# Optimization experiments

Hardware: AMD Instinct MI355X
Metric: run time of the kernel (lower is better)

The kernel has to match this reference:

```python
import jax, jax.numpy as jnp
import numpy as np

N_CONN = 21  # n_connections


def setup_inputs() -> dict:
    key = jax.random.key(0)
    landmarks = jax.random.normal(key, (262144, N_CONN, 3), dtype=jnp.float32)
    return {"landmarks": landmarks}


def reference(landmarks) -> jnp.ndarray:
    # Faithful to the TF layer: connections = [(i, j) for i in range(n) for j in range(n)],
    # connection_vectors[k] = landmarks[:, j_k] - landmarks[:, i_k]; the loop only reads
    # indices k < n, which correspond to pairs (0, k), so v_k = p_k - p_0 (v_0 == 0).
    b, n = landmarks.shape[0], N_CONN
    v = landmarks[:, :n, :] - landmarks[:, :1, :]          # (b, n, d)
    dots = jnp.einsum("bid,bjd->bij", v, v)                 # (b, n, n)
    norms = jnp.linalg.norm(v, axis=-1)                     # (b, n)
    cos = dots / (norms[:, :, None] * norms[:, None, :])    # 0/0 -> nan for v_0
    ang = jnp.arccos(cos)                                   # (b, n, n)
    ang = jnp.where(jnp.isnan(ang), jnp.zeros_like(ang), ang)
    # TF concatenates n*n tensors of shape (batch,) along axis -1 (== axis 0),
    # yielding shape (n*n*batch,) ordered angle-major.
    return ang.reshape(b, n * n).T.reshape(-1)
```

## Files before the change

### kernel.cpp

```cpp
#include <hip/hip_runtime.h>

#define NCONN 21

typedef float f4 __attribute__((ext_vector_type(4)));

__device__ __forceinline__ float acos_poly(float c) {
    c = fmaxf(fminf(c, 1.0f), -1.0f);
    float t = fabsf(c);
    float s = sqrtf(1.0f - t);
    float p = fmaf(t, -0.0187293f, 0.0742610f);
    p = fmaf(t, p, -0.2121144f);
    p = fmaf(t, p, 1.5707288f);
    float r = s * p;
    return (c >= 0.0f) ? r : (3.14159265358979f - r);
}

__global__ __launch_bounds__(256, 2) void k1_planes(const float* __restrict__ in,
                                                    float* __restrict__ ws, int B) {
    __shared__ float lds[256 * 64];
    const int tid = threadIdx.x;
    const long long blockBatch = (long long)blockIdx.x * 256;

    const long long gBase4 = blockBatch * 63 / 4;
    const float4* in4 = (const float4*)in;
    #pragma unroll
    for (int it = 0; it < 16; ++it) {
        int t4 = tid + it * 256;
        if (t4 < 4032) {
            float4 v = in4[gBase4 + t4];
            float vals[4] = {v.x, v.y, v.z, v.w};
            int f = 4 * t4;
            #pragma unroll
            for (int q = 0; q < 4; ++q) {
                int f2 = f + q;
                int r  = f2 / 63;
                int c  = f2 - r * 63;
                lds[r * 64 + ((c + (r >> 2)) & 63)] = vals[q];
            }
        }
    }
    __syncthreads();

    {
        float* row = lds + tid * 64;
        const int rot = tid >> 2;
        const float p0x = row[(0 + rot) & 63];
        const float p0y = row[(1 + rot) & 63];
        const float p0z = row[(2 + rot) & 63];
        #pragma unroll
        for (int e = 1; e < NCONN; ++e) {
            const int s0 = (3 * e + 0 + rot) & 63;
            const int s1 = (3 * e + 1 + rot) & 63;
            const int s2 = (3 * e + 2 + rot) & 63;
            float vx = row[s0] - p0x;
            float vy = row[s1] - p0y;
            float vz = row[s2] - p0z;
            float d  = fmaf(vx, vx, fmaf(vy, vy, vz * vz));
            float rr = rsqrtf(d);
            row[s0] = vx * rr;
            row[s1] = vy * rr;
            row[s2] = vz * rr;
        }
    }
    __syncthreads();

    const int l = tid & 63, w = tid >> 6;
    const int rowb = 4 * l;
    for (int q = w; q < 60; q += 4) {
        f4 val;
        #pragma unroll
        for (int k = 0; k < 4; ++k)
            val[k] = lds[(rowb + k) * 64 + ((q + 3 + l) & 63)];
        *(f4*)(ws + (size_t)q * B + blockBatch + rowb) = val;
    }
}

#define SPAN 1024
__global__ __launch_bounds__(256) void k2_rows(const float* __restrict__ ws,
                                               float* __restrict__ out, int B) {
    const int tid = threadIdx.x;
    const int l = tid & 63;
    const int W = blockIdx.x * 4 + (tid >> 6);
    const int unit = W % 11;
    const int sp = W / 11;
    const long long b0 = (long long)sp * SPAN;
    const size_t sB = (size_t)B;
    const f4 z4 = {0.f, 0.f, 0.f, 0.f};

    for (int ch = 0; ch < SPAN / 256; ++ch) {
        const long long lb = b0 + ch * 256 + 4 * l;
        if (unit == 10) {
            for (int j = 0; j < NCONN; ++j)
                __builtin_nontemporal_store(z4, (f4*)(out + (size_t)j * sB + lb));
        } else {
            const int i0 = 2 * unit + 1, i1 = i0 + 1;
            const float* pw = ws + lb;
            const f4 ax = *(const f4*)(pw + (size_t)(3 * (i0 - 1) + 0) * sB);
            const f4 ay = *(const f4*)(pw + (size_t)(3 * (i0 - 1) + 1) * sB);
            const f4 az = *(const f4*)(pw + (size_t)(3 * (i0 - 1) + 2) * sB);
            const f4 bx = *(const f4*)(pw + (size_t)(3 * (i1 - 1) + 0) * sB);
            const f4 by = *(const f4*)(pw + (size_t)(3 * (i1 - 1) + 1) * sB);
            const f4 bz = *(const f4*)(pw + (size_t)(3 * (i1 - 1) + 2) * sB);
            __builtin_nontemporal_store(z4, (f4*)(out + (size_t)(i0 * NCONN) * sB + lb));
            __builtin_nontemporal_store(z4, (f4*)(out + (size_t)(i1 * NCONN) * sB + lb));
            for (int j = 1; j < NCONN; ++j) {
                const f4 jx = *(const f4*)(pw + (size_t)(3 * (j - 1) + 0) * sB);
                const f4 jy = *(const f4*)(pw + (size_t)(3 * (j - 1) + 1) * sB);
                const f4 jz = *(const f4*)(pw + (size_t)(3 * (j - 1) + 2) * sB);
                f4 a0, a1;
                #pragma unroll
                for (int k = 0; k < 4; ++k) {
                    a0[k] = acos_poly(fmaf(ax[k], jx[k], fmaf(ay[k], jy[k], az[k] * jz[k])));
                    a1[k] = acos_poly(fmaf(bx[k], jx[k], fmaf(by[k], jy[k], bz[k] * jz[k])));
                }
                __builtin_nontemporal_store(a0, (f4*)(out + (size_t)(i0 * NCONN + j) * sB + lb));
                __builtin_nontemporal_store(a1, (f4*)(out + (size_t)(i1 * NCONN + j) * sB + lb));
            }
        }
    }
}

#define FTPB 512
#define FBPB 256
__global__ __launch_bounds__(FTPB, 4) void pv_fallback(const float* __restrict__ in,
                                                       float* __restrict__ out,
                                                       int B) {
    __shared__ float lds[FBPB * 64];
    const int tid = threadIdx.x;
    const long long blockBatch = (long long)blockIdx.x * FBPB;

    const long long gBase4 = blockBatch * 63 / 4;
    const long long totalF4 = ((long long)B * 63) >> 2;
    const float4* in4 = (const float4*)in;
    #pragma unroll
    for (int it = 0; it < 8; ++it) {
        int t4 = tid + it * FTPB;
        if (t4 < (FBPB * 63) / 4) {
            long long g4 = gBase4 + t4;
            if (g4 < totalF4) {
                float4 v = in4[g4];
                float vals[4] = {v.x, v.y, v.z, v.w};
                int f = 4 * t4;
                #pragma unroll
                for (int q = 0; q < 4; ++q) {
                    int f2 = f + q;
                    int r  = f2 / 63;
                    int c  = f2 - r * 63;
                    lds[r * 64 + ((c + (r >> 2)) & 63)] = vals[q];
                }
            }
        }
    }
    __syncthreads();

    if (tid < FBPB && blockBatch + tid < B) {
        float* row = lds + tid * 64;
        const int rot = tid >> 2;
        const float p0x = row[(0 + rot) & 63];
        const float p0y = row[(1 + rot) & 63];
        const float p0z = row[(2 + rot) & 63];
        #pragma unroll
        for (int e = 1; e < NCONN; ++e) {
            const int s0 = (3 * e + 0 + rot) & 63;
            const int s1 = (3 * e + 1 + rot) & 63;
            const int s2 = (3 * e + 2 + rot) & 63;
            float vx = row[s0] - p0x;
            float vy = row[s1] - p0y;
            float vz = row[s2] - p0z;
            float d  = fmaf(vx, vx, fmaf(vy, vy, vz * vz));
            float rr = rsqrtf(d);
            row[s0] = vx * rr;
            row[s1] = vy * rr;
            row[s2] = vz * rr;
        }
    }
    __syncthreads();

    const int l = tid & 63;
    const int w = tid >> 6;
    const int rowb = 4 * l;
    const long long remLL = B - blockBatch;
    const int rem = (int)(remLL < FBPB ? remLL : (long long)FBPB);
    const bool fullv = (rowb + 4 <= rem);
    float* op = out + blockBatch + rowb;
    const size_t sB = (size_t)B;

    {
        const f4 z4 = {0.f, 0.f, 0.f, 0.f};
        for (int idx = w; idx < 41; idx += 8) {
            const int p = (idx < 21) ? idx : (idx - 20) * NCONN;
            float* dst = op + (size_t)p * sB;
            if (fullv) __builtin_nontemporal_store(z4, (f4*)dst);
            else for (int k = 0; rowb + k < rem; ++k) dst[k] = 0.0f;
        }
    }

    for (int idx = w; idx < 400; idx += 8) {
        const int i = idx / 20 + 1;
        const int j = idx - (i - 1) * 20 + 1;
        f4 ang;
        #pragma unroll
        for (int k = 0; k < 4; ++k) {
            const float* row = lds + (rowb + k) * 64;
            const float uix = row[(3 * i + 0 + l) & 63];
            const float uiy = row[(3 * i + 1 + l) & 63];
            const float uiz = row[(3 * i + 2 + l) & 63];
            const float ujx = row[(3 * j + 0 + l) & 63];
            const float ujy = row[(3 * j + 1 + l) & 63];
            const float ujz = row[(3 * j + 2 + l) & 63];
            ang[k] = acos_poly(fmaf(uix, ujx, fmaf(uiy, ujy, uiz * ujz)));
        }
        float* dst = op + (size_t)(i * NCONN + j) * sB;
        if (fullv) __builtin_nontemporal_store(ang, (f4*)dst);
        else for (int k = 0; rowb + k < rem; ++k) dst[k] = ang[k];
    }
}

extern "C" void kernel_launch(void* const* d_in, const int* in_sizes, int n_in,
                              void* d_out, int out_size, void* d_ws, size_t ws_size,
                              hipStream_t stream) {
    const float* in = (const float*)d_in[0];
    float* out = (float*)d_out;
    const int B = in_sizes[0] / (NCONN * 3);
    const size_t needWS = (size_t)60 * (size_t)B * sizeof(float);

    if (ws_size >= needWS && (B % 4096) == 0) {
        float* ws = (float*)d_ws;
        hipLaunchKernelGGL(k1_planes, dim3(B / 256), dim3(256), 0, stream, in, ws, B);
        const int waves = 11 * (B / SPAN);
        hipLaunchKernelGGL(k2_rows, dim3(waves / 4), dim3(256), 0, stream, ws, out, B);
    } else {
        const int grid = (B + FBPB - 1) / FBPB;
        hipLaunchKernelGGL(pv_fallback, dim3(grid), dim3(FTPB), 0, stream, in, out, B);
    }
}
```

Before: 544.0 us.

## Restructure angle kernel so each thread computes four rows per j-plane load

```diff
diff --git a/kernel.cpp b/kernel.cpp
--- a/kernel.cpp
+++ b/kernel.cpp
@@ -75,47 +75,55 @@
     }
 }
 
-#define SPAN 1024
-__global__ __launch_bounds__(256) void k2_rows(const float* __restrict__ ws,
-                                               float* __restrict__ out, int B) {
+__global__ __launch_bounds__(256) void k2_sweep(const float* __restrict__ ws,
+                                                float* __restrict__ out, int B) {
+    const int NS = B >> 10;
+    const int g = blockIdx.x / NS;
+    const int s = blockIdx.x - g * NS;
     const int tid = threadIdx.x;
-    const int l = tid & 63;
-    const int W = blockIdx.x * 4 + (tid >> 6);
-    const int unit = W % 11;
-    const int sp = W / 11;
-    const long long b0 = (long long)sp * SPAN;
+    const long long b0 = ((long long)s << 10) + 4 * tid;
     const size_t sB = (size_t)B;
+    float* po = out + b0;
     const f4 z4 = {0.f, 0.f, 0.f, 0.f};
 
-    for (int ch = 0; ch < SPAN / 256; ++ch) {
-        const long long lb = b0 + ch * 256 + 4 * l;
-        if (unit == 10) {
-            for (int j = 0; j < NCONN; ++j)
-                __builtin_nontemporal_store(z4, (f4*)(out + (size_t)j * sB + lb));
-        } else {
-            const int i0 = 2 * unit + 1, i1 = i0 + 1;
-            const float* pw = ws + lb;
-            const f4 ax = *(const f4*)(pw + (size_t)(3 * (i0 - 1) + 0) * sB);
-            const f4 ay = *(const f4*)(pw + (size_t)(3 * (i0 - 1) + 1) * sB);
-            const f4 az = *(const f4*)(pw + (size_t)(3 * (i0 - 1) + 2) * sB);
-            const f4 bx = *(const f4*)(pw + (size_t)(3 * (i1 - 1) + 0) * sB);
-            const f4 by = *(const f4*)(pw + (size_t)(3 * (i1 - 1) + 1) * sB);
-            const f4 bz = *(const f4*)(pw + (size_t)(3 * (i1 - 1) + 2) * sB);
-            __builtin_nontemporal_store(z4, (f4*)(out + (size_t)(i0 * NCONN) * sB + lb));
-            __builtin_nontemporal_store(z4, (f4*)(out + (size_t)(i1 * NCONN) * sB + lb));
-            for (int j = 1; j < NCONN; ++j) {
-                const f4 jx = *(const f4*)(pw + (size_t)(3 * (j - 1) + 0) * sB);
-                const f4 jy = *(const f4*)(pw + (size_t)(3 * (j - 1) + 1) * sB);
-                const f4 jz = *(const f4*)(pw + (size_t)(3 * (j - 1) + 2) * sB);
-                f4 a0, a1;
-                #pragma unroll
-                for (int k = 0; k < 4; ++k) {
-                    a0[k] = acos_poly(fmaf(ax[k], jx[k], fmaf(ay[k], jy[k], az[k] * jz[k])));
-                    a1[k] = acos_poly(fmaf(bx[k], jx[k], fmaf(by[k], jy[k], bz[k] * jz[k])));
-                }
-                __builtin_nontemporal_store(a0, (f4*)(out + (size_t)(i0 * NCONN + j) * sB + lb));
-                __builtin_nontemporal_store(a1, (f4*)(out + (size_t)(i1 * NCONN + j) * sB + lb));
+    if (g == 5) {
+        #pragma unroll
+        for (int p = 0; p < NCONN; ++p)
+            __builtin_nontemporal_store(z4, (f4*)(po + (size_t)p * sB));
+        return;
+    }
+
+    const float* pw = ws + b0;
+    f4 ix[4], iy[4], iz[4];
+    #pragma unroll
+    for (int k = 0; k < 4; ++k) {
+        const int q = 3 * (4 * g + k);
+        ix[k] = *(const f4*)(pw + (size_t)(q + 0) * sB);
+        iy[k] = *(const f4*)(pw + (size_t)(q + 1) * sB);
+        iz[k] = *(const f4*)(pw + (size_t)(q + 2) * sB);
+    }
+
+    #pragma unroll
+    for (int k = 0; k < 4; ++k) {
+        const int i = 4 * g + 1 + k;
+        __builtin_nontemporal_store(z4, (f4*)(po + (size_t)(i * NCONN) * sB));
+    }
+
+    for (int j = 1; j < NCONN; ++j) {
+        const int q = 3 * (j - 1);
+        const f4 jx = *(const f4*)(pw + (size_t)(q + 0) * sB);
+        const f4 jy = *(const f4*)(pw + (size_t)(q + 1) * sB);
+        const f4 jz = *(const f4*)(pw + (size_t)(q + 2) * sB);
+        #pragma unroll
+        for (int k = 0; k < 4; ++k) {
+            const int i = 4 * g + 1 + k;
+            f4 ang;
+            #pragma unroll
+            for (int e = 0; e < 4; ++e) {
+                float c = fmaf(ix[k][e], jx[e], fmaf(iy[k][e], jy[e], iz[k][e] * jz[e]));
+                ang[e] = acos_poly(c);
             }
+            __builtin_nontemporal_store(ang, (f4*)(po + (size_t)(i * NCONN + j) * sB));
         }
     }
 }
@@ -224,11 +232,11 @@
     const int B = in_sizes[0] / (NCONN * 3);
     const size_t needWS = (size_t)60 * (size_t)B * sizeof(float);
 
-    if (ws_size >= needWS && (B % 4096) == 0) {
+    if (ws_size >= needWS && (B % 1024) == 0) {
         float* ws = (float*)d_ws;
         hipLaunchKernelGGL(k1_planes, dim3(B / 256), dim3(256), 0, stream, in, ws, B);
-        const int waves = 11 * (B / SPAN);
-        hipLaunchKernelGGL(k2_rows, dim3(waves / 4), dim3(256), 0, stream, ws, out, B);
+        const int NS = B >> 10;
+        hipLaunchKernelGGL(k2_sweep, dim3(6 * NS), dim3(256), 0, stream, ws, out, B);
     } else {
         const int grid = (B + FBPB - 1) / FBPB;
         hipLaunchKernelGGL(pv_fallback, dim3(grid), dim3(FTPB), 0, stream, in, out, B);
```

Measured after the change: 534.7 us. No clear change (-1.7%).
